# Optimization experiments

Hardware: AMD Instinct MI355X
Metric: run time of the kernel (lower is better)

## Reference

```python
import jax, jax.numpy as jnp
import numpy as np

T, B, D, H = 512, 64, 512, 512  # seq_len, batch, input_size, hidden_size


def setup_inputs() -> dict:
    key = jax.random.key(0)
    ks = jax.random.split(key, 7)
    s = jnp.float32(0.05)  # keep gates out of saturation
    return {
        "x": jax.random.normal(ks[0], (T, B, D), jnp.float32),
        "Wi_l0": jax.random.normal(ks[1], (2, 4 * H, D), jnp.float32) * s,
        "Wh_l0": jax.random.normal(ks[2], (2, 4 * H, H), jnp.float32) * s,
        "b_l0": jax.random.normal(ks[3], (2, 4 * H), jnp.float32) * s,
        "Wi_l1": jax.random.normal(ks[4], (2, 4 * H, 2 * H), jnp.float32) * s,
        "Wh_l1": jax.random.normal(ks[5], (2, 4 * H, H), jnp.float32) * s,
        "b_l1": jax.random.normal(ks[6], (2, 4 * H), jnp.float32) * s,
    }


def _lstm_dir(xs, Wi, Wh, b):
    """Run one LSTM direction over xs: [T, B, Din] -> ([T, B, H], h_T, c_T)."""
    Bsz = xs.shape[1]
    Hh = Wh.shape[-1]
    # Precompute input contribution for all timesteps (the big GEMM).
    gx = jnp.einsum('tbd,gd->tbg', xs, Wi) + b  # [T, B, 4H]

    def step(carry, gx_t):
        h, c = carry
        gates = gx_t + h @ Wh.T  # [B, 4H]
        i, f, g, o = jnp.split(gates, 4, axis=-1)
        c = jax.nn.sigmoid(f) * c + jax.nn.sigmoid(i) * jnp.tanh(g)
        h = jax.nn.sigmoid(o) * jnp.tanh(c)
        return (h, c), h

    h0 = jnp.zeros((Bsz, Hh), xs.dtype)
    (hT, cT), hs = jax.lax.scan(step, (h0, h0), gx)
    return hs, hT, cT


def _bilstm_layer(xs, Wi, Wh, b):
    hf, hTf, cTf = _lstm_dir(xs, Wi[0], Wh[0], b[0])
    hb, hTb, cTb = _lstm_dir(xs[::-1], Wi[1], Wh[1], b[1])
    # torch.stack(dim=2).view(T, B, -1) == concat along feature axis
    out = jnp.concatenate([hf, hb[::-1]], axis=-1)  # [T, B, 2H]
    return out, (hTf, hTb), (cTf, cTb)


def reference(x, Wi_l0, Wh_l0, b_l0, Wi_l1, Wh_l1, b_l1):
    o0, h0s, c0s = _bilstm_layer(x, Wi_l0, Wh_l0, b_l0)
    o1, h1s, c1s = _bilstm_layer(o0, Wi_l1, Wh_l1, b_l1)
    # state order: (layer0 fwd, layer0 bwd, layer1 fwd, layer1 bwd)
    h_n = jnp.stack(h0s + h1s, axis=0)  # [4, B, H]
    c_n = jnp.stack(c0s + c1s, axis=0)  # [4, B, H]
    return o1, (h_n, c_n)
```

## Files before the change

kernel.cpp:

```cpp
#include <hip/hip_runtime.h>
#include <stdint.h>


#define TT 512
#define BATCH 64
#define HH 512
#define NWG 64
#define NCOLS 32

typedef __attribute__((ext_vector_type(8))) short vshort8;
typedef __attribute__((ext_vector_type(4))) float vfloat4;

__device__ __forceinline__ vfloat4 mfma16(vshort8 a, vshort8 b, vfloat4 c) {
    return __builtin_amdgcn_mfma_f32_16x16x32_bf16(a, b, c, 0, 0, 0);
}

__device__ __forceinline__ float sigmoidf_(float x) {
    return 1.f / (1.f + __expf(-x));
}
__device__ __forceinline__ float tanhf_(float x) {
    float e = __expf(2.f * x);
    return 1.f - 2.f / (e + 1.f);
}
__device__ __forceinline__ unsigned short f2bf(float f) {
    uint32_t u = __float_as_uint(f);
    uint32_t r = (u + 0x7fffu + ((u >> 16) & 1u)) >> 16;
    return (unsigned short)r;
}

__global__ void cvt_f32_bf16(const float* __restrict__ src,
                             unsigned short* __restrict__ dst, int n) {
    int i = (blockIdx.x * blockDim.x + threadIdx.x) * 4;
    if (i + 3 < n) {
        float4 v = *(const float4*)(src + i);
        uint2 p;
        p.x = (uint32_t)f2bf(v.x) | ((uint32_t)f2bf(v.y) << 16);
        p.y = (uint32_t)f2bf(v.z) | ((uint32_t)f2bf(v.w) << 16);
        *(uint2*)(dst + i) = p;
    }
}

template <int DIN, bool WRITE_BF16>
__launch_bounds__(256, 1)
__global__ void lstm_phase(const unsigned short* __restrict__ A,
                           const unsigned short* __restrict__ Wi,
                           const unsigned short* __restrict__ Wh,
                           const float* __restrict__ bias,
                           unsigned short* __restrict__ hbuf,
                           int* __restrict__ flags,
                           unsigned short* __restrict__ obf,
                           float* __restrict__ of32,
                           float* __restrict__ hn,
                           float* __restrict__ cn)
{
    __shared__ unsigned short Wlds[NCOLS * DIN];
    __shared__ unsigned short Whlds[NCOLS * HH];

    const int tid = threadIdx.x;
    const int dir = blockIdx.x >> 6;
    const int wg = blockIdx.x & 63;
    const int j0 = wg * 8;
    const int lane = tid & 63;
    const int wave = tid >> 6;

    for (int chunk = tid; chunk < NCOLS * DIN / 8; chunk += 256) {
        int n = chunk / (DIN / 8);
        int k8 = (chunk % (DIN / 8)) * 8;
        int grow = (n >> 3) * HH + j0 + (n & 7);
        vshort8 v = *(const vshort8*)(Wi + ((size_t)dir * 4 * HH + grow) * DIN + k8);
        int byte = n * DIN * 2 + ((k8 * 2) ^ ((n & 7) << 4));
        *(vshort8*)((char*)Wlds + byte) = v;
    }
    for (int chunk = tid; chunk < NCOLS * HH / 8; chunk += 256) {
        int n = chunk / (HH / 8);
        int k8 = (chunk % (HH / 8)) * 8;
        int grow = (n >> 3) * HH + j0 + (n & 7);
        vshort8 v = *(const vshort8*)(Wh + ((size_t)dir * 4 * HH + grow) * HH + k8);
        int byte = n * HH * 2 + ((k8 * 2) ^ ((n & 7) << 4));
        *(vshort8*)((char*)Whlds + byte) = v;
    }
    __syncthreads();

    const int arow = wave * 16 + (lane & 15);
    const int kOff = (lane >> 4) * 8;
    const int klane = (lane >> 4) * 16;
    const int n0 = lane & 15;
    const int swz = (n0 & 7) << 4;
    const int nb0 = n0 * DIN * 2;
    const int nb1 = (16 + n0) * DIN * 2;
    const int nb0h = n0 * HH * 2;
    const int nb1h = (16 + n0) * HH * 2;
    const int grow0 = (n0 >> 3) * HH + j0 + (n0 & 7);
    const int grow1 = ((n0 >> 3) + 2) * HH + j0 + (n0 & 7);
    const float bias0 = bias[dir * 4 * HH + grow0];
    const float bias1 = bias[dir * 4 * HH + grow1];
    const bool lo = (lane & 8) == 0;
    const int j = lane & 7;
    const int jcol = j0 + j;
    const int hrowb = wave * 16 + ((lane >> 4) << 2);

    float cstate[4] = {0.f, 0.f, 0.f, 0.f};

    for (int s = 0; s < TT; ++s) {
        const int t = dir ? (TT - 1 - s) : s;

        vfloat4 acc0, acc1;
        acc0[0] = acc0[1] = acc0[2] = acc0[3] = bias0;
        acc1[0] = acc1[1] = acc1[2] = acc1[3] = bias1;

        const unsigned short* ap = A + ((size_t)t * BATCH + arow) * DIN + kOff;
#pragma unroll 8
        for (int kk = 0; kk < DIN / 32; ++kk) {
            vshort8 a = *(const vshort8*)(ap + kk * 32);
            int kb = kk * 64 + klane;
            vshort8 b0 = *(const vshort8*)((const char*)Wlds + nb0 + (kb ^ swz));
            vshort8 b1 = *(const vshort8*)((const char*)Wlds + nb1 + (kb ^ swz));
            acc0 = mfma16(a, b0, acc0);
            acc1 = mfma16(a, b1, acc1);
        }

        if (s > 0) {
            if (wave == 0) {
                const int* slotp = flags + dir * NWG + lane;
                for (;;) {
                    int v;
                    asm volatile(
                        "global_load_dword %0, %1, off sc0 sc1\n\t"
                        "s_waitcnt vmcnt(0)"
                        : "=v"(v) : "v"(slotp) : "memory");
                    if (!__any(v < s)) break;
                    __builtin_amdgcn_s_sleep(1);
                }
            }
            __syncthreads();

            const unsigned short* hp =
                hbuf + (((dir << 1) | ((s - 1) & 1)) * BATCH + arow) * HH + kOff;
            vshort8 ha[HH / 32];
#pragma unroll
            for (int kk = 0; kk < HH / 32; ++kk)
                asm volatile("global_load_dwordx4 %0, %1, off sc0 sc1"
                             : "=v"(ha[kk]) : "v"(hp + kk * 32) : "memory");
            asm volatile("s_waitcnt vmcnt(0)" ::: "memory");
            __builtin_amdgcn_sched_barrier(0);
#pragma unroll
            for (int kk = 0; kk < HH / 32; ++kk) {
                int kb = kk * 64 + klane;
                vshort8 b0 = *(const vshort8*)((const char*)Whlds + nb0h + (kb ^ swz));
                vshort8 b1 = *(const vshort8*)((const char*)Whlds + nb1h + (kb ^ swz));
                acc0 = mfma16(ha[kk], b0, acc0);
                acc1 = mfma16(ha[kk], b1, acc1);
            }
        }

        float hval[4];
#pragma unroll
        for (int r = 0; r < 4; ++r) {
            float own0 = acc0[r], own1 = acc1[r];
            float oth0 = __shfl_xor(own0, 8, 64);
            float oth1 = __shfl_xor(own1, 8, 64);
            float iv = lo ? own0 : oth0;
            float fv = lo ? oth0 : own0;
            float gv = lo ? own1 : oth1;
            float ov = lo ? oth1 : own1;
            float cnew = sigmoidf_(fv) * cstate[r] + sigmoidf_(iv) * tanhf_(gv);
            cstate[r] = cnew;
            hval[r] = sigmoidf_(ov) * tanhf_(cnew);
        }

        unsigned short* hw = hbuf + (size_t)(((dir << 1) | (s & 1)) * BATCH) * HH;
        const int rA = lo ? 0 : 2;
#pragma unroll
        for (int q = 0; q < 2; ++q) {
            int r = rA + q, row = hrowb + r;
            unsigned short hb = f2bf(hval[r]);
            unsigned short* hwp = hw + row * HH + jcol;
            uint32_t hb32 = hb;
            asm volatile("global_store_short %0, %1, off sc0 sc1"
                         :: "v"(hwp), "v"(hb32) : "memory");
            if constexpr (WRITE_BF16)
                obf[((size_t)t * BATCH + row) * (2 * HH) + dir * HH + jcol] = hb;
            else
                of32[((size_t)t * BATCH + row) * (2 * HH) + dir * HH + jcol] = hval[r];
        }
        if (s == TT - 1) {
#pragma unroll
            for (int q = 0; q < 2; ++q) {
                int r = rA + q, row = hrowb + r;
                hn[(dir * BATCH + row) * HH + jcol] = hval[r];
                cn[(dir * BATCH + row) * HH + jcol] = cstate[r];
            }
        }

        asm volatile("s_waitcnt vmcnt(0)" ::: "memory");
        __syncthreads();
        if (tid == 0) {
            int* myslot = flags + dir * NWG + wg;
            int ep = s + 1;
            asm volatile("global_store_dword %0, %1, off sc0 sc1"
                         :: "v"(myslot), "v"(ep) : "memory");
        }
    }
}

extern "C" void kernel_launch(void* const* d_in, const int* in_sizes, int n_in,
                              void* d_out, int out_size, void* d_ws, size_t ws_size,
                              hipStream_t stream) {
    const float* x = (const float*)d_in[0];
    const float* Wi0 = (const float*)d_in[1];
    const float* Wh0 = (const float*)d_in[2];
    const float* b0 = (const float*)d_in[3];
    const float* Wi1 = (const float*)d_in[4];
    const float* Wh1 = (const float*)d_in[5];
    const float* b1 = (const float*)d_in[6];

    char* ws = (char*)d_ws;
    int* flags = (int*)(ws + 0);
    unsigned short* hbuf = (unsigned short*)(ws + 8192);
    unsigned short* wi0b = (unsigned short*)(ws + 270336);
    unsigned short* wh0b = (unsigned short*)(ws + 4464640);
    unsigned short* wi1b = (unsigned short*)(ws + 8658944);
    unsigned short* wh1b = (unsigned short*)(ws + 17047552);
    unsigned short* xb = (unsigned short*)(ws + 21241856);
    unsigned short* o0 = (unsigned short*)(ws + 54796288);

    float* out = (float*)d_out;
    const size_t O1SZ = (size_t)TT * BATCH * 2 * HH;
    float* hn_base = out + O1SZ;
    float* cn_base = out + O1SZ + 4 * BATCH * HH;

    hipMemsetAsync(flags, 0, 1024, stream);

    {
        int n;
        n = TT * BATCH * 512;
        cvt_f32_bf16<<<n / 1024, 256, 0, stream>>>(x, xb, n);
        n = 2 * 2048 * 512;
        cvt_f32_bf16<<<n / 1024, 256, 0, stream>>>(Wi0, wi0b, n);
        cvt_f32_bf16<<<n / 1024, 256, 0, stream>>>(Wh0, wh0b, n);
        cvt_f32_bf16<<<n / 1024, 256, 0, stream>>>(Wh1, wh1b, n);
        n = 2 * 2048 * 1024;
        cvt_f32_bf16<<<n / 1024, 256, 0, stream>>>(Wi1, wi1b, n);
    }

    lstm_phase<512, true><<<128, 256, 0, stream>>>(
        xb, wi0b, wh0b, b0, hbuf, flags, o0, nullptr, hn_base, cn_base);

    lstm_phase<1024, false><<<128, 256, 0, stream>>>(
        o0, wi1b, wh1b, b1, hbuf, flags + 2 * NWG, nullptr, out,
        hn_base + 2 * BATCH * HH, cn_base + 2 * BATCH * HH);
}
```

Baseline: 7.528 ms.

## Keep recurrent weights in registers and replace block barriers with per-wave flags

The recurrent weight slice Wh now lives in VGPRs, loaded once before the time loop. It was previously staged in LDS and re-read every step, so this removes the per-step LDS reads of Wh. The cross-workgroup handshake becomes per wave: each wave publishes its own flag and polls the matching wave's flags in the other workgroups, with no sleep. This removes the two __syncthreads per step and the wave-0 gate, so each wave waits only on the batch rows it depends on. The cost is much higher register pressure, a flag array four times larger, and more polling traffic to global memory.

```diff
diff --git a/kernel.cpp b/kernel.cpp
--- a/kernel.cpp
+++ b/kernel.cpp
@@ -54,7 +54,6 @@
                            float* __restrict__ cn)
 {
     __shared__ unsigned short Wlds[NCOLS * DIN];
-    __shared__ unsigned short Whlds[NCOLS * HH];
 
     const int tid = threadIdx.x;
     const int dir = blockIdx.x >> 6;
@@ -71,14 +70,6 @@
         int byte = n * DIN * 2 + ((k8 * 2) ^ ((n & 7) << 4));
         *(vshort8*)((char*)Wlds + byte) = v;
     }
-    for (int chunk = tid; chunk < NCOLS * HH / 8; chunk += 256) {
-        int n = chunk / (HH / 8);
-        int k8 = (chunk % (HH / 8)) * 8;
-        int grow = (n >> 3) * HH + j0 + (n & 7);
-        vshort8 v = *(const vshort8*)(Wh + ((size_t)dir * 4 * HH + grow) * HH + k8);
-        int byte = n * HH * 2 + ((k8 * 2) ^ ((n & 7) << 4));
-        *(vshort8*)((char*)Whlds + byte) = v;
-    }
     __syncthreads();
 
     const int arow = wave * 16 + (lane & 15);
@@ -88,8 +79,6 @@
     const int swz = (n0 & 7) << 4;
     const int nb0 = n0 * DIN * 2;
     const int nb1 = (16 + n0) * DIN * 2;
-    const int nb0h = n0 * HH * 2;
-    const int nb1h = (16 + n0) * HH * 2;
     const int grow0 = (n0 >> 3) * HH + j0 + (n0 & 7);
     const int grow1 = ((n0 >> 3) + 2) * HH + j0 + (n0 & 7);
     const float bias0 = bias[dir * 4 * HH + grow0];
@@ -98,6 +87,15 @@
     const int j = lane & 7;
     const int jcol = j0 + j;
     const int hrowb = wave * 16 + ((lane >> 4) << 2);
+
+    const unsigned short* whp0 = Wh + ((size_t)dir * 4 * HH + grow0) * HH + kOff;
+    const unsigned short* whp1 = Wh + ((size_t)dir * 4 * HH + grow1) * HH + kOff;
+    vshort8 wh0r[16], wh1r[16];
+#pragma unroll
+    for (int kk = 0; kk < 16; ++kk) {
+        wh0r[kk] = *(const vshort8*)(whp0 + kk * 32);
+        wh1r[kk] = *(const vshort8*)(whp1 + kk * 32);
+    }
 
     float cstate[4] = {0.f, 0.f, 0.f, 0.f};
 
@@ -120,36 +118,29 @@
         }
 
         if (s > 0) {
-            if (wave == 0) {
-                const int* slotp = flags + dir * NWG + lane;
-                for (;;) {
-                    int v;
-                    asm volatile(
-                        "global_load_dword %0, %1, off sc0 sc1\n\t"
-                        "s_waitcnt vmcnt(0)"
-                        : "=v"(v) : "v"(slotp) : "memory");
-                    if (!__any(v < s)) break;
-                    __builtin_amdgcn_s_sleep(1);
-                }
+            const int* slotp = flags + ((dir * NWG + lane) << 2) + wave;
+            for (;;) {
+                int v;
+                asm volatile(
+                    "global_load_dword %0, %1, off sc0 sc1\n\t"
+                    "s_waitcnt vmcnt(0)"
+                    : "=v"(v) : "v"(slotp) : "memory");
+                if (!__any(v < s)) break;
             }
-            __syncthreads();
 
             const unsigned short* hp =
                 hbuf + (((dir << 1) | ((s - 1) & 1)) * BATCH + arow) * HH + kOff;
-            vshort8 ha[HH / 32];
-#pragma unroll
-            for (int kk = 0; kk < HH / 32; ++kk)
+            vshort8 ha[16];
+#pragma unroll
+            for (int kk = 0; kk < 16; ++kk)
                 asm volatile("global_load_dwordx4 %0, %1, off sc0 sc1"
                              : "=v"(ha[kk]) : "v"(hp + kk * 32) : "memory");
             asm volatile("s_waitcnt vmcnt(0)" ::: "memory");
             __builtin_amdgcn_sched_barrier(0);
 #pragma unroll
-            for (int kk = 0; kk < HH / 32; ++kk) {
-                int kb = kk * 64 + klane;
-                vshort8 b0 = *(const vshort8*)((const char*)Whlds + nb0h + (kb ^ swz));
-                vshort8 b1 = *(const vshort8*)((const char*)Whlds + nb1h + (kb ^ swz));
-                acc0 = mfma16(ha[kk], b0, acc0);
-                acc1 = mfma16(ha[kk], b1, acc1);
+            for (int kk = 0; kk < 16; ++kk) {
+                acc0 = mfma16(ha[kk], wh0r[kk], acc0);
+                acc1 = mfma16(ha[kk], wh1r[kk], acc1);
             }
         }
 
@@ -193,9 +184,9 @@
         }
 
         asm volatile("s_waitcnt vmcnt(0)" ::: "memory");
-        __syncthreads();
-        if (tid == 0) {
-            int* myslot = flags + dir * NWG + wg;
+        __builtin_amdgcn_sched_barrier(0);
+        if (lane == 0) {
+            int* myslot = flags + ((dir * NWG + wg) << 2) + wave;
             int ep = s + 1;
             asm volatile("global_store_dword %0, %1, off sc0 sc1"
                          :: "v"(myslot), "v"(ep) : "memory");
@@ -229,7 +220,7 @@
     float* hn_base = out + O1SZ;
     float* cn_base = out + O1SZ + 4 * BATCH * HH;
 
-    hipMemsetAsync(flags, 0, 1024, stream);
+    hipMemsetAsync(flags, 0, 4096, stream);
 
     {
         int n;
@@ -247,6 +238,6 @@
         xb, wi0b, wh0b, b0, hbuf, flags, o0, nullptr, hn_base, cn_base);
 
     lstm_phase<1024, false><<<128, 256, 0, stream>>>(
-        o0, wi1b, wh1b, b1, hbuf, flags + 2 * NWG, nullptr, out,
+        o0, wi1b, wh1b, b1, hbuf, flags + 512, nullptr, out,
         hn_base + 2 * BATCH * HH, cn_base + 2 * BATCH * HH);
 }
```

Result: slower. 8.543 ms (+13.5%).

## Replace per-step flag barrier with tagged hidden-state words polled by consumers

Applied to the files above, without the earlier changes.

The kernel no longer uses a separate per-workgroup flag array. Each hidden value is now stored as a 32-bit word holding the bf16 value plus a 16-bit step tag. Consumers poll a sentinel word, then reload their whole h tile until every tag matches before running the recurrent MFMAs. This removes the vmcnt drain, __syncthreads and flag store on the producer side and the wave-0 poll plus block barrier on the consumer side, at the cost of doubling h-buffer traffic and possibly retrying full reloads. The two Wh conversion kernels are also dropped, with fp32-to-bf16 conversion folded into the LDS preload.

```diff
diff --git a/kernel.cpp b/kernel.cpp
--- a/kernel.cpp
+++ b/kernel.cpp
@@ -10,6 +10,7 @@
 
 typedef __attribute__((ext_vector_type(8))) short vshort8;
 typedef __attribute__((ext_vector_type(4))) float vfloat4;
+typedef __attribute__((ext_vector_type(4))) unsigned int vuint4;
 
 __device__ __forceinline__ vfloat4 mfma16(vshort8 a, vshort8 b, vfloat4 c) {
     return __builtin_amdgcn_mfma_f32_16x16x32_bf16(a, b, c, 0, 0, 0);
@@ -44,10 +45,9 @@
 __launch_bounds__(256, 1)
 __global__ void lstm_phase(const unsigned short* __restrict__ A,
                            const unsigned short* __restrict__ Wi,
-                           const unsigned short* __restrict__ Wh,
+                           const float* __restrict__ Whf,
                            const float* __restrict__ bias,
-                           unsigned short* __restrict__ hbuf,
-                           int* __restrict__ flags,
+                           uint32_t* __restrict__ hbuf32,
                            unsigned short* __restrict__ obf,
                            float* __restrict__ of32,
                            float* __restrict__ hn,
@@ -75,7 +75,14 @@
         int n = chunk / (HH / 8);
         int k8 = (chunk % (HH / 8)) * 8;
         int grow = (n >> 3) * HH + j0 + (n & 7);
-        vshort8 v = *(const vshort8*)(Wh + ((size_t)dir * 4 * HH + grow) * HH + k8);
+        const float* src = Whf + ((size_t)dir * 4 * HH + grow) * HH + k8;
+        float4 f0 = *(const float4*)(src);
+        float4 f1 = *(const float4*)(src + 4);
+        vshort8 v;
+        v[0] = (short)f2bf(f0.x); v[1] = (short)f2bf(f0.y);
+        v[2] = (short)f2bf(f0.z); v[3] = (short)f2bf(f0.w);
+        v[4] = (short)f2bf(f1.x); v[5] = (short)f2bf(f1.y);
+        v[6] = (short)f2bf(f1.z); v[7] = (short)f2bf(f1.w);
         int byte = n * HH * 2 + ((k8 * 2) ^ ((n & 7) << 4));
         *(vshort8*)((char*)Whlds + byte) = v;
     }
@@ -95,9 +102,9 @@
     const float bias0 = bias[dir * 4 * HH + grow0];
     const float bias1 = bias[dir * 4 * HH + grow1];
     const bool lo = (lane & 8) == 0;
-    const int j = lane & 7;
-    const int jcol = j0 + j;
+    const int jcol = j0 + (lane & 7);
     const int hrowb = wave * 16 + ((lane >> 4) << 2);
+    const int scol = (lane & 15) * 32 + (lane >> 4) * 8;
 
     float cstate[4] = {0.f, 0.f, 0.f, 0.f};
 
@@ -120,36 +127,53 @@
         }
 
         if (s > 0) {
-            if (wave == 0) {
-                const int* slotp = flags + dir * NWG + lane;
-                for (;;) {
-                    int v;
-                    asm volatile(
-                        "global_load_dword %0, %1, off sc0 sc1\n\t"
-                        "s_waitcnt vmcnt(0)"
-                        : "=v"(v) : "v"(slotp) : "memory");
-                    if (!__any(v < s)) break;
-                    __builtin_amdgcn_s_sleep(1);
-                }
-            }
-            __syncthreads();
-
-            const unsigned short* hp =
-                hbuf + (((dir << 1) | ((s - 1) & 1)) * BATCH + arow) * HH + kOff;
-            vshort8 ha[HH / 32];
-#pragma unroll
-            for (int kk = 0; kk < HH / 32; ++kk)
-                asm volatile("global_load_dwordx4 %0, %1, off sc0 sc1"
-                             : "=v"(ha[kk]) : "v"(hp + kk * 32) : "memory");
-            asm volatile("s_waitcnt vmcnt(0)" ::: "memory");
+            const uint32_t* rowbase =
+                hbuf32 + (((dir << 1) | ((s - 1) & 1)) * BATCH + arow) * HH;
+            const uint32_t* rbase = rowbase + kOff;
+            const uint32_t want = (uint32_t)s;
+
+            for (;;) {
+                uint32_t sent;
+                asm volatile(
+                    "global_load_dword %0, %1, off sc0 sc1\n\t"
+                    "s_waitcnt vmcnt(0)"
+                    : "=v"(sent) : "v"(rowbase + scol) : "memory");
+                if (!__any(((sent ^ want) & 0xffffu) != 0)) break;
+                __builtin_amdgcn_s_sleep(1);
+            }
+
+            vuint4 hd[32];
+            for (;;) {
+#pragma unroll
+                for (int q = 0; q < 32; ++q)
+                    asm volatile("global_load_dwordx4 %0, %1, off sc0 sc1"
+                                 : "=v"(hd[q])
+                                 : "v"(rbase + (q >> 1) * 32 + (q & 1) * 4));
+                asm volatile("s_waitcnt vmcnt(0)" ::: "memory");
+                __builtin_amdgcn_sched_barrier(0);
+                uint32_t diff = 0;
+#pragma unroll
+                for (int q = 0; q < 32; ++q)
+                    diff |= (hd[q][0] ^ want) | (hd[q][1] ^ want) |
+                            (hd[q][2] ^ want) | (hd[q][3] ^ want);
+                if (!__any((diff & 0xffffu) != 0)) break;
+                __builtin_amdgcn_s_sleep(1);
+            }
             __builtin_amdgcn_sched_barrier(0);
-#pragma unroll
-            for (int kk = 0; kk < HH / 32; ++kk) {
+
+#pragma unroll
+            for (int kk = 0; kk < 16; ++kk) {
+                uint32_t d0 = __builtin_amdgcn_perm(hd[2 * kk][1], hd[2 * kk][0], 0x07060302u);
+                uint32_t d1 = __builtin_amdgcn_perm(hd[2 * kk][3], hd[2 * kk][2], 0x07060302u);
+                uint32_t d2 = __builtin_amdgcn_perm(hd[2 * kk + 1][1], hd[2 * kk + 1][0], 0x07060302u);
+                uint32_t d3 = __builtin_amdgcn_perm(hd[2 * kk + 1][3], hd[2 * kk + 1][2], 0x07060302u);
+                vuint4 tt = {d0, d1, d2, d3};
+                vshort8 ha = __builtin_bit_cast(vshort8, tt);
                 int kb = kk * 64 + klane;
                 vshort8 b0 = *(const vshort8*)((const char*)Whlds + nb0h + (kb ^ swz));
                 vshort8 b1 = *(const vshort8*)((const char*)Whlds + nb1h + (kb ^ swz));
-                acc0 = mfma16(ha[kk], b0, acc0);
-                acc1 = mfma16(ha[kk], b1, acc1);
+                acc0 = mfma16(ha, b0, acc0);
+                acc1 = mfma16(ha, b1, acc1);
             }
         }
 
@@ -168,16 +192,17 @@
             hval[r] = sigmoidf_(ov) * tanhf_(cnew);
         }
 
-        unsigned short* hw = hbuf + (size_t)(((dir << 1) | (s & 1)) * BATCH) * HH;
+        uint32_t* hw = hbuf32 + (size_t)(((dir << 1) | (s & 1)) * BATCH) * HH;
         const int rA = lo ? 0 : 2;
+        const uint32_t tagv = (uint32_t)(s + 1);
 #pragma unroll
         for (int q = 0; q < 2; ++q) {
             int r = rA + q, row = hrowb + r;
             unsigned short hb = f2bf(hval[r]);
-            unsigned short* hwp = hw + row * HH + jcol;
-            uint32_t hb32 = hb;
-            asm volatile("global_store_short %0, %1, off sc0 sc1"
-                         :: "v"(hwp), "v"(hb32) : "memory");
+            uint32_t val = ((uint32_t)hb << 16) | tagv;
+            uint32_t* wp = hw + row * HH + jcol;
+            asm volatile("global_store_dword %0, %1, off sc0 sc1"
+                         :: "v"(wp), "v"(val) : "memory");
             if constexpr (WRITE_BF16)
                 obf[((size_t)t * BATCH + row) * (2 * HH) + dir * HH + jcol] = hb;
             else
@@ -190,15 +215,6 @@
                 hn[(dir * BATCH + row) * HH + jcol] = hval[r];
                 cn[(dir * BATCH + row) * HH + jcol] = cstate[r];
             }
-        }
-
-        asm volatile("s_waitcnt vmcnt(0)" ::: "memory");
-        __syncthreads();
-        if (tid == 0) {
-            int* myslot = flags + dir * NWG + wg;
-            int ep = s + 1;
-            asm volatile("global_store_dword %0, %1, off sc0 sc1"
-                         :: "v"(myslot), "v"(ep) : "memory");
         }
     }
 }
@@ -215,21 +231,19 @@
     const float* b1 = (const float*)d_in[6];
 
     char* ws = (char*)d_ws;
-    int* flags = (int*)(ws + 0);
-    unsigned short* hbuf = (unsigned short*)(ws + 8192);
-    unsigned short* wi0b = (unsigned short*)(ws + 270336);
-    unsigned short* wh0b = (unsigned short*)(ws + 4464640);
-    unsigned short* wi1b = (unsigned short*)(ws + 8658944);
-    unsigned short* wh1b = (unsigned short*)(ws + 17047552);
-    unsigned short* xb = (unsigned short*)(ws + 21241856);
-    unsigned short* o0 = (unsigned short*)(ws + 54796288);
+    uint32_t* hbufA = (uint32_t*)(ws);
+    uint32_t* hbufB = (uint32_t*)(ws + 524288);
+    unsigned short* wi0b = (unsigned short*)(ws + 1048576);
+    unsigned short* wi1b = (unsigned short*)(ws + 5242880);
+    unsigned short* xb = (unsigned short*)(ws + 13631488);
+    unsigned short* o0 = (unsigned short*)(ws + 47185920);
 
     float* out = (float*)d_out;
     const size_t O1SZ = (size_t)TT * BATCH * 2 * HH;
     float* hn_base = out + O1SZ;
     float* cn_base = out + O1SZ + 4 * BATCH * HH;
 
-    hipMemsetAsync(flags, 0, 1024, stream);
+    hipMemsetAsync(hbufA, 0, 1048576, stream);
 
     {
         int n;
@@ -237,16 +251,14 @@
         cvt_f32_bf16<<<n / 1024, 256, 0, stream>>>(x, xb, n);
         n = 2 * 2048 * 512;
         cvt_f32_bf16<<<n / 1024, 256, 0, stream>>>(Wi0, wi0b, n);
-        cvt_f32_bf16<<<n / 1024, 256, 0, stream>>>(Wh0, wh0b, n);
-        cvt_f32_bf16<<<n / 1024, 256, 0, stream>>>(Wh1, wh1b, n);
         n = 2 * 2048 * 1024;
         cvt_f32_bf16<<<n / 1024, 256, 0, stream>>>(Wi1, wi1b, n);
     }
 
     lstm_phase<512, true><<<128, 256, 0, stream>>>(
-        xb, wi0b, wh0b, b0, hbuf, flags, o0, nullptr, hn_base, cn_base);
+        xb, wi0b, Wh0, b0, hbufA, o0, nullptr, hn_base, cn_base);
 
     lstm_phase<1024, false><<<128, 256, 0, stream>>>(
-        o0, wi1b, wh1b, b1, hbuf, flags + 2 * NWG, nullptr, out,
+        o0, wi1b, Wh1, b1, hbufB, nullptr, out,
         hn_base + 2 * BATCH * HH, cn_base + 2 * BATCH * HH);
 }
```

Result: slower. 8.105 ms (+7.7%).
